# Optimization experiments

Hardware: AMD Instinct MI355X
Metric: run time of the kernel (lower is better)

## Reference

```python
import jax, jax.numpy as jnp
import numpy as np

D_MODEL, D_STATE, D_CONV, EXPAND, L = 512, 16, 4, 2, 2048
D_INNER = EXPAND * D_MODEL


def _dwconv_causal(x, w, b):
    # x: (L, D), w: (D, K), b: (D,). torch Conv1d(groups=D, padding=K-1)[..., :L]
    K = w.shape[1]
    xp = jnp.pad(x, ((K - 1, 0), (0, 0)))
    windows = jnp.stack([xp[k:k + x.shape[0]] for k in range(K)], axis=-1)  # (L, D, K)
    return jnp.einsum('ldk,dk->ld', windows, w) + b


def _ssm_dir(x, inW, inb, cw, cb, xpW, xpb, dtW, dtb, outW, outb, A_log, Dp):
    xz = x @ inW + inb                      # (L, 2*Di)
    x_ssm, z = xz[:, :D_INNER], xz[:, D_INNER:]
    x_ssm = _dwconv_causal(x_ssm, cw, cb)   # (L, Di)
    sp = jax.nn.silu(x_ssm) @ xpW + xpb     # (L, Di + 2*S)
    delta = sp[:, :D_INNER]
    B = sp[:, D_INNER:D_INNER + D_STATE]
    C = sp[:, D_INNER + D_STATE:]
    dt = jax.nn.softplus(delta @ dtW + dtb)  # (L, Di)
    A = -jnp.exp(A_log)                      # (Di, S)
    dA = jnp.exp(dt[:, :, None] * A[None])                      # (L, Di, S)
    dBu = dt[:, :, None] * B[:, None, :] * x_ssm[:, :, None]    # (L, Di, S)

    def step(h, inp):
        a, bu = inp
        h = a * h + bu
        return h, h

    h0 = jnp.zeros((D_INNER, D_STATE), x.dtype)
    _, hs = jax.lax.scan(step, h0, (dA, dBu))   # (L, Di, S)
    y = jnp.einsum('lds,ls->ld', hs, C) + Dp * x_ssm
    return (y * jax.nn.silu(z)) @ outW + outb


def _make_params(key):
    ks = jax.random.split(key, 32)
    i = iter(range(32))
    def w(shape, scale=0.02):
        return (jax.random.normal(ks[next(i)], shape, jnp.float32) * scale)
    p = {}
    for pre in ('fwd_', 'bwd_'):
        p[pre + 'in_W'] = w((D_MODEL, 2 * D_INNER))
        p[pre + 'in_b'] = w((2 * D_INNER,))
        p[pre + 'conv_w'] = w((D_INNER, D_CONV), 0.1)
        p[pre + 'conv_b'] = w((D_INNER,))
        p[pre + 'xp_W'] = w((D_INNER, D_INNER + 2 * D_STATE))
        p[pre + 'xp_b'] = w((D_INNER + 2 * D_STATE,))
        p[pre + 'dt_W'] = w((D_INNER, D_INNER))
        p[pre + 'dt_b'] = w((D_INNER,))
        p[pre + 'out_W'] = w((D_INNER, D_MODEL))
        p[pre + 'out_b'] = w((D_MODEL,))
    p['A_log'] = jax.random.normal(ks[next(i)], (D_INNER, D_STATE), jnp.float32) * 0.5
    p['D_param'] = jnp.ones((D_INNER,), jnp.float32)
    p['fusion_W'] = w((2 * D_MODEL, D_MODEL))
    p['fusion_b'] = w((D_MODEL,))
    return p


def setup_inputs() -> dict:
    key = jax.random.key(0)
    kx, kp = jax.random.split(key)
    inp = {'x': jax.random.normal(kx, (L, D_MODEL), jnp.float32)}
    inp.update(_make_params(kp))
    return inp


def reference(x,
              fwd_in_W, fwd_in_b, fwd_conv_w, fwd_conv_b, fwd_xp_W, fwd_xp_b,
              fwd_dt_W, fwd_dt_b, fwd_out_W, fwd_out_b,
              bwd_in_W, bwd_in_b, bwd_conv_w, bwd_conv_b, bwd_xp_W, bwd_xp_b,
              bwd_dt_W, bwd_dt_b, bwd_out_W, bwd_out_b,
              A_log, D_param, fusion_W, fusion_b):
    out_fwd = _ssm_dir(x, fwd_in_W, fwd_in_b, fwd_conv_w, fwd_conv_b,
                       fwd_xp_W, fwd_xp_b, fwd_dt_W, fwd_dt_b,
                       fwd_out_W, fwd_out_b, A_log, D_param)
    out_bwd = _ssm_dir(x[::-1], bwd_in_W, bwd_in_b, bwd_conv_w, bwd_conv_b,
                       bwd_xp_W, bwd_xp_b, bwd_dt_W, bwd_dt_b,
                       bwd_out_W, bwd_out_b, A_log, D_param)[::-1]
    return jnp.concatenate([out_fwd, out_bwd], axis=-1) @ fusion_W + fusion_b
```

## Files before the change

### kernel.cpp

```cpp
#include <hip/hip_runtime.h>
#include <cmath>

#define L_SEQ 2048
#define DM 512
#define DI 1024
#define DS 16
#define NSP 1056
#define NC 64
#define CL 32

typedef unsigned short ushortT;
typedef unsigned int u32;
typedef __attribute__((ext_vector_type(8))) short short8;
typedef __attribute__((ext_vector_type(4))) unsigned short ushort4_t;
typedef __attribute__((ext_vector_type(4))) float float4_t;
typedef __attribute__((address_space(1))) u32 gu32;
typedef __attribute__((address_space(3))) u32 lu32;

__device__ __forceinline__ float sigm(float x) { return 1.0f / (1.0f + __expf(-x)); }

__device__ __forceinline__ ushortT f2bf(float f) {
    unsigned u = __float_as_uint(f);
    unsigned r = u + 0x7FFFu + ((u >> 16) & 1u);
    return (ushortT)(r >> 16);
}
__device__ __forceinline__ float b2f(ushortT u) {
    return __uint_as_float(((u32)u) << 16);
}

__device__ __forceinline__ void gl2lds16(const ushortT* g, ushortT* l) {
    __builtin_amdgcn_global_load_lds((gu32*)g, (lu32*)l, 16, 0, 0);
}

struct WC {
    const float* src[11];
    ushortT* dst[11];
    int ss[11], soff[11], ds_[11], tN[11], mode[11];
    int off[12];
};

__global__ __launch_bounds__(256) void prep_all(
    WC wc, int nW,
    const float* __restrict__ x, ushortT* __restrict__ xb,
    const float* __restrict__ xpb0, const float* __restrict__ xpb1,
    const float* __restrict__ dtW0, const float* __restrict__ dtW1,
    const float* __restrict__ dtb0, const float* __restrict__ dtb1,
    const float* __restrict__ outb0, const float* __restrict__ outb1,
    const float* __restrict__ fuW, const float* __restrict__ fub,
    float* __restrict__ BFdt0, float* __restrict__ BFdt1, float* __restrict__ BFof)
{
    __shared__ ushortT t[32][33];
    __shared__ float red[256];
    int b = blockIdx.x;
    int tid = threadIdx.x;
    if (b < nW) {
        int m = 0;
        while (b >= wc.off[m + 1]) ++m;
        int tl = b - wc.off[m];
        int n0 = (tl % wc.tN[m]) * 32;
        int k0 = (tl / wc.tN[m]) * 32;
        const float* W = wc.src[m];
        ushortT* D = wc.dst[m];
        int ss = wc.ss[m], soff = wc.soff[m], ds = wc.ds_[m];
        int tx = tid & 31, ty = tid >> 5;
        if (wc.mode[m] == 1) {
            #pragma unroll
            for (int i = 0; i < 32; i += 8)
                D[(size_t)(k0 + ty + i) * ds + n0 + tx] =
                    f2bf(W[(size_t)(k0 + ty + i) * ss + soff + n0 + tx]);
        } else {
            #pragma unroll
            for (int i = 0; i < 32; i += 8)
                t[ty + i][tx] = f2bf(W[(size_t)(k0 + ty + i) * ss + soff + n0 + tx]);
            __syncthreads();
            #pragma unroll
            for (int i = 0; i < 32; i += 8)
                D[(size_t)(n0 + ty + i) * ds + k0 + tx] = t[tx][ty + i];
        }
        return;
    }
    b -= nW;
    if (b < 1024) {
        int i = (b * 256 + tid) * 4;
        float4_t v = *(const float4_t*)(x + i);
        xb[i + 0] = f2bf(v[0]); xb[i + 1] = f2bf(v[1]);
        xb[i + 2] = f2bf(v[2]); xb[i + 3] = f2bf(v[3]);
        return;
    }
    int o = b - 1024;
    float acc = 0.0f;
    if (o < 2112) {
        int dir = o >= 1056;
        int m = o - dir * 1056;
        const float* xpb = dir ? xpb1 : xpb0;
        float* BF = dir ? BFdt1 : BFdt0;
        if (m >= 1024) {
            if (tid == 0) BF[m] = xpb[m];
            return;
        }
        const float* dtW = dir ? dtW1 : dtW0;
        const float* dtb = dir ? dtb1 : dtb0;
        for (int n = tid; n < 1024; n += 256) acc += xpb[n] * dtW[n * 1024 + m];
        red[tid] = acc;
        __syncthreads();
        for (int s = 128; s > 0; s >>= 1) {
            if (tid < s) red[tid] += red[tid + s];
            __syncthreads();
        }
        if (tid == 0) BF[m] = red[0] + dtb[m];
    } else {
        int n = o - 2112;
        for (int j = tid; j < 1024; j += 256) {
            float ob = (j < 512) ? outb0[j] : outb1[j - 512];
            acc += ob * fuW[(size_t)j * 512 + n];
        }
        red[tid] = acc;
        __syncthreads();
        for (int s = 128; s > 0; s >>= 1) {
            if (tid < s) red[tid] += red[tid + s];
            __syncthreads();
        }
        if (tid == 0) BFof[n] = red[0] + fub[n];
    }
}

template<int BM, int BN>
__device__ __forceinline__ void gemm_core(
    ushortT* As, ushortT* Bs, int bm, int bn,
    const ushortT* __restrict__ A, int lda, int revA,
    const ushortT* __restrict__ A2, int dualK,
    const ushortT* __restrict__ W,
    const float* __restrict__ bias,
    float* __restrict__ Cf, int ldcf,
    float* __restrict__ Cf2, int ldcf2, int Nsplit,
    ushortT* __restrict__ Cb, int ldcb,
    ushortT* __restrict__ Cb2, int ldcb2,
    int M, int N, int K, int epi)
{
    constexpr int BK = 64;
    constexpr int MI = BM / 32;
    constexpr int NI = BN / 32;
    constexpr int CA = BM / 32;
    constexpr int CB = BN / 32;
    constexpr int ABUF = BM * BK;
    constexpr int BBUF = BN * BK;

    const int tid  = threadIdx.x;
    const int wave = tid >> 6;
    const int lane = tid & 63;
    const int quad = lane >> 4;
    const int r    = lane & 15;
    const int wm   = (wave >> 1) * (BM / 2);
    const int wn   = (wave & 1) * (BN / 2);

    const int lrow = lane >> 3;
    const int lk   = ((lane & 7) ^ lrow) * 8;

    const ushortT* gA[CA]; const ushortT* gA2[CA]; ushortT* lA[CA];
    #pragma unroll
    for (int c = 0; c < CA; ++c) {
        int row = bm + c * 32 + wave * 8 + lrow;
        int r0 = revA ? (M - 1 - row) : row;
        gA[c] = A + (size_t)r0 * lda + lk;
        gA2[c] = dualK ? (A2 + (size_t)(M - 1 - row) * lda + lk) : gA[c];
        lA[c] = &As[(c * 32 + wave * 8) * BK];
    }
    const ushortT* gB[CB]; ushortT* lB[CB];
    #pragma unroll
    for (int c = 0; c < CB; ++c) {
        int row = bn + c * 32 + wave * 8 + lrow;
        if (row > N - 1) row = N - 1;
        gB[c] = W + (size_t)row * K + lk;
        lB[c] = &Bs[(c * 32 + wave * 8) * BK];
    }

    float4_t acc[MI][NI];
    #pragma unroll
    for (int i = 0; i < MI; ++i)
        #pragma unroll
        for (int j = 0; j < NI; ++j)
            acc[i][j] = (float4_t){0.f, 0.f, 0.f, 0.f};

    const int nsteps = K >> 6;

    auto stage = [&](int step, int buf) {
        int kq = step << 6;
        #pragma unroll
        for (int c = 0; c < CA; ++c) {
            const ushortT* s = (!dualK || kq < 1024) ? gA[c] + kq : gA2[c] + (kq - 1024);
            gl2lds16(s, lA[c] + buf * ABUF);
        }
        #pragma unroll
        for (int c = 0; c < CB; ++c)
            gl2lds16(gB[c] + kq, lB[c] + buf * BBUF);
    };
    auto compute = [&](int buf) {
        #pragma unroll
        for (int kh = 0; kh < 2; ++kh) {
            const int slot = (((kh * 4 + quad) ^ (lane & 7)) * 8);
            short8 af[MI], bf[NI];
            #pragma unroll
            for (int mi = 0; mi < MI; ++mi)
                af[mi] = *(const short8*)&As[buf * ABUF + (wm + mi * 16 + r) * BK + slot];
            #pragma unroll
            for (int ni = 0; ni < NI; ++ni)
                bf[ni] = *(const short8*)&Bs[buf * BBUF + (wn + ni * 16 + r) * BK + slot];
            #pragma unroll
            for (int mi = 0; mi < MI; ++mi)
                #pragma unroll
                for (int ni = 0; ni < NI; ++ni)
                    acc[mi][ni] = __builtin_amdgcn_mfma_f32_16x16x32_bf16(
                        af[mi], bf[ni], acc[mi][ni], 0, 0, 0);
        }
    };

    stage(0, 0);
    for (int i = 0; i < nsteps; i += 2) {
        __syncthreads();
        if (i + 1 < nsteps) stage(i + 1, 1);
        compute(0);
        __syncthreads();
        if (i + 2 < nsteps) stage(i + 2, 0);
        compute(1);
    }

    #pragma unroll
    for (int mi = 0; mi < MI; ++mi) {
        int rowb = bm + wm + mi * 16 + quad * 4;
        #pragma unroll
        for (int ni = 0; ni < NI; ++ni) {
            int gn = bn + wn + ni * 16 + r;
            if (gn < N) {
                float bv = bias ? bias[gn] : 0.0f;
                #pragma unroll
                for (int j = 0; j < 4; ++j) {
                    int orow = rowb + j;
                    float v = acc[mi][ni][j] + bv;
                    if (gn < Nsplit) {
                        if (epi == 1) v = (v > 20.0f) ? v : log1pf(__expf(v));
                        if (Cf) Cf[(size_t)orow * ldcf + gn] = v;
                        if (Cb) Cb[(size_t)orow * ldcb + gn] = f2bf(v);
                    } else {
                        if (Cf2) Cf2[(size_t)orow * ldcf2 + gn - Nsplit] = v;
                        if (Cb2) Cb2[(size_t)orow * ldcb2 + gn - Nsplit] = f2bf(v);
                    }
                }
            }
        }
    }
}

__global__ __launch_bounds__(256) void mega_k(
    const ushortT* __restrict__ XB, const ushortT* __restrict__ WtIn,
    const float* __restrict__ inb0, const float* __restrict__ inb1,
    ushortT* __restrict__ XSb, ushortT* __restrict__ Zb,
    const ushortT* __restrict__ WtDt, const ushortT* __restrict__ XpD,
    ushortT* __restrict__ WtXpF,
    const ushortT* __restrict__ WtFu, const ushortT* __restrict__ OutC,
    ushortT* __restrict__ WtOF2)
{
    __shared__ ushortT As[2 * 128 * 64];
    __shared__ ushortT Bs[2 * 64 * 64];
    int z = blockIdx.z;
    if (z < 2) {
        long long b = ((long long)z * 16 + blockIdx.y) * 32 + blockIdx.x;
        int xc = (int)(b & 7);
        long long k = b >> 3;
        int dir = xc & 1;
        int q = xc >> 1;
        int bx = q * 8 + (int)(k % 8);
        int by = (int)(k / 8);
        gemm_core<128, 64>(As, Bs, by * 128, bx * 64,
            XB, DM, dir, nullptr, 0,
            WtIn + (size_t)dir * 2 * DI * DM,
            dir ? inb1 : inb0,
            nullptr, 0, nullptr, 0, DI,
            XSb + (size_t)dir * L_SEQ * DI, DI,
            Zb + (size_t)dir * L_SEQ * DI, DI,
            L_SEQ, 2 * DI, DM, 0);
    } else if (z < 4) {
        if (blockIdx.x >= 16) return;
        int d = z - 2;
        gemm_core<64, 64>(As, Bs, blockIdx.y * 64, blockIdx.x * 64,
            WtDt + (size_t)d * DI * DI, DI, 0, nullptr, 0,
            XpD + (size_t)d * DI * DI,
            nullptr, nullptr, 0, nullptr, 0, DI,
            WtXpF + (size_t)d * NSP * DI, DI, nullptr, 0,
            DI, DI, DI, 0);
    } else {
        if (blockIdx.x >= 16 || blockIdx.y >= 8) return;
        int d = z - 4;
        gemm_core<64, 64>(As, Bs, blockIdx.y * 64, blockIdx.x * 64,
            WtFu + (size_t)d * DM, DI, 0, nullptr, 0,
            OutC + (size_t)d * DI * DM,
            nullptr, nullptr, 0, nullptr, 0, DI,
            WtOF2 + (size_t)d * DI, 2 * DI, nullptr, 0,
            DM, DI, DM, 0);
    }
}

template<int BM, int BN>
__global__ __launch_bounds__(256) void gemm_bf16(
    const ushortT* __restrict__ A, int lda, long long Astr, int revAmode,
    const ushortT* __restrict__ W, long long Wstr,
    const float* __restrict__ bias0, const float* __restrict__ bias1,
    float* __restrict__ Cf, int ldcf, long long Cfstr,
    float* __restrict__ Cf2, int ldcf2, long long Cf2str, int Nsplit,
    ushortT* __restrict__ Cb, int ldcb, long long Cbstr,
    ushortT* __restrict__ Cb2, int ldcb2, long long Cb2str,
    int swz, int M, int N, int K, int epi)
{
    __shared__ ushortT As[2 * BM * 64];
    __shared__ ushortT Bs[2 * BN * 64];
    int bx = blockIdx.x, by = blockIdx.y, dir = blockIdx.z;
    if (swz) {
        int gx = gridDim.x, gy = gridDim.y, gz = gridDim.z;
        long long b = ((long long)dir * gy + by) * gx + bx;
        int xc = (int)(b & 7);
        long long k = b >> 3;
        if (gz == 2) {
            dir = xc & 1;
            int q = xc >> 1;
            if (swz == 1) { int qc = gx >> 2; bx = q * qc + (int)(k % qc); by = (int)(k / qc); }
            else          { int qc = gy >> 2; by = q * qc + (int)(k % qc); bx = (int)(k / qc); }
        } else {
            if (swz == 1) { int qc = gx >> 3; bx = xc * qc + (int)(k % qc); by = (int)(k / qc); }
            else          { int qc = gy >> 3; by = xc * qc + (int)(k % qc); bx = (int)(k / qc); }
        }
    }
    const ushortT* Ad = A;
    const ushortT* A2 = A;
    int revA = 0, dualK = 0;
    if (revAmode == 3) { dualK = 1; A2 = A + Astr; }
    else { Ad += (size_t)dir * Astr; revA = (revAmode == 2) ? dir : revAmode; }
    gemm_core<BM, BN>(As, Bs, by * BM, bx * BN,
        Ad, lda, revA, A2, dualK,
        W + (size_t)dir * Wstr,
        dir ? bias1 : bias0,
        Cf ? Cf + (size_t)dir * Cfstr : nullptr, ldcf,
        Cf2 ? Cf2 + (size_t)dir * Cf2str : nullptr, ldcf2, Nsplit,
        Cb ? Cb + (size_t)dir * Cbstr : nullptr, ldcb,
        Cb2 ? Cb2 + (size_t)dir * Cb2str : nullptr, ldcb2,
        M, N, K, epi);
}

__global__ __launch_bounds__(256) void conv_k(
    const ushortT* __restrict__ XSb,
    const float* __restrict__ cw0, const float* __restrict__ cw1,
    const float* __restrict__ cb0, const float* __restrict__ cb1,
    ushortT* __restrict__ SCb)
{
    int dir = blockIdx.z;
    XSb += (size_t)dir * L_SEQ * DI;
    SCb += (size_t)dir * L_SEQ * DI;
    const float* cw = dir ? cw1 : cw0;
    const float* cb = dir ? cb1 : cb0;
    int idx = (blockIdx.x * 256 + threadIdx.x) * 4;
    int d4 = idx & (DI - 1);
    int l = idx >> 10;
    ushort4_t r0 = *(const ushort4_t*)(XSb + (size_t)l * DI + d4);
    ushort4_t r1 = (l >= 1) ? *(const ushort4_t*)(XSb + (size_t)(l - 1) * DI + d4) : (ushort4_t){0,0,0,0};
    ushort4_t r2 = (l >= 2) ? *(const ushort4_t*)(XSb + (size_t)(l - 2) * DI + d4) : (ushort4_t){0,0,0,0};
    ushort4_t r3 = (l >= 3) ? *(const ushort4_t*)(XSb + (size_t)(l - 3) * DI + d4) : (ushort4_t){0,0,0,0};
    ushort4_t outv;
    #pragma unroll
    for (int j = 0; j < 4; ++j) {
        int d = d4 + j;
        float acc = cb[d] + cw[d * 4 + 0] * b2f(r3[j]) + cw[d * 4 + 1] * b2f(r2[j])
                  + cw[d * 4 + 2] * b2f(r1[j]) + cw[d * 4 + 3] * b2f(r0[j]);
        outv[j] = f2bf(acc * sigm(acc));
    }
    *(ushort4_t*)(SCb + idx) = outv;
}

__global__ __launch_bounds__(256) void scanA_k(
    const ushortT* __restrict__ DTb, const ushortT* __restrict__ XSb,
    const float* __restrict__ BC, const float* __restrict__ Alog,
    const float* __restrict__ cw0, const float* __restrict__ cw1,
    const float* __restrict__ cb0, const float* __restrict__ cb1,
    float* __restrict__ Pend, float* __restrict__ Hl)
{
    __shared__ float Bsh[CL][DS];
    int dir = blockIdx.z;
    int c = blockIdx.y;
    int d = blockIdx.x * 256 + threadIdx.x;
    DTb += (size_t)dir * L_SEQ * DI;
    XSb += (size_t)dir * L_SEQ * DI;
    BC  += (size_t)dir * L_SEQ * 32;
    const float* cw = dir ? cw1 : cw0;
    const float* cb = dir ? cb1 : cb0;
    int l0 = c * CL;
    for (int i = threadIdx.x; i < CL * DS; i += 256) {
        int ll = i >> 4, ss = i & 15;
        Bsh[ll][ss] = BC[(size_t)(l0 + ll) * 32 + ss];
    }
    __syncthreads();
    float w0 = cw[d * 4 + 0], w1 = cw[d * 4 + 1], w2 = cw[d * 4 + 2], w3 = cw[d * 4 + 3];
    float cbv = cb[d];
    float x3 = (l0 >= 3) ? b2f(XSb[(size_t)(l0 - 3) * DI + d]) : 0.f;
    float x2 = (l0 >= 2) ? b2f(XSb[(size_t)(l0 - 2) * DI + d]) : 0.f;
    float x1 = (l0 >= 1) ? b2f(XSb[(size_t)(l0 - 1) * DI + d]) : 0.f;
    float Ae[DS], h[DS], P[DS];
    #pragma unroll
    for (int s = 0; s < DS; ++s) { Ae[s] = -__expf(Alog[d * DS + s]); h[s] = 0.f; P[s] = 1.f; }
    for (int t = 0; t < CL; ++t) {
        int l = l0 + t;
        float x0 = b2f(XSb[(size_t)l * DI + d]);
        float xv = cbv + w0 * x3 + w1 * x2 + w2 * x1 + w3 * x0;
        x3 = x2; x2 = x1; x1 = x0;
        float dt = b2f(DTb[(size_t)l * DI + d]);
        float dtx = dt * xv;
        #pragma unroll
        for (int s = 0; s < DS; ++s) {
            float e = __expf(dt * Ae[s]);
            h[s] = e * h[s] + dtx * Bsh[t][s];
            P[s] *= e;
        }
    }
    size_t o = ((size_t)(dir * NC + c) * DI + d) * DS;
    #pragma unroll
    for (int s = 0; s < DS; ++s) { Pend[o + s] = P[s]; Hl[o + s] = h[s]; }
}

__global__ __launch_bounds__(256) void scanB_k(
    const float* __restrict__ Pend, const float* __restrict__ Hl, float* __restrict__ Hs)
{
    int idx = blockIdx.x * 256 + threadIdx.x;
    float h = 0.f;
    int ds = idx & 16383;
    int dir = idx >> 14;
    for (int c = 0; c < NC; ++c) {
        size_t o = ((size_t)(dir * NC + c)) * (DI * DS) + ds;
        Hs[o] = h;
        h = Pend[o] * h + Hl[o];
    }
}

__global__ __launch_bounds__(256) void scanC_k(
    const ushortT* __restrict__ DTb, const ushortT* __restrict__ XSb,
    const float* __restrict__ BC, const ushortT* __restrict__ Zb,
    const float* __restrict__ Alog, const float* __restrict__ Dp,
    const float* __restrict__ cw0, const float* __restrict__ cw1,
    const float* __restrict__ cb0, const float* __restrict__ cb1,
    const float* __restrict__ Hs, ushortT* __restrict__ Gb)
{
    __shared__ float Bsh[CL][DS];
    __shared__ float Csh[CL][DS];
    int dir = blockIdx.z;
    int c = blockIdx.y;
    int d = blockIdx.x * 256 + threadIdx.x;
    DTb += (size_t)dir * L_SEQ * DI;
    XSb += (size_t)dir * L_SEQ * DI;
    BC  += (size_t)dir * L_SEQ * 32;
    Zb  += (size_t)dir * L_SEQ * DI;
    Gb  += (size_t)dir * L_SEQ * DI;
    const float* cw = dir ? cw1 : cw0;
    const float* cb = dir ? cb1 : cb0;
    int l0 = c * CL;
    for (int i = threadIdx.x; i < CL * DS; i += 256) {
        int ll = i >> 4, ss = i & 15;
        size_t base = (size_t)(l0 + ll) * 32;
        Bsh[ll][ss] = BC[base + ss];
        Csh[ll][ss] = BC[base + DS + ss];
    }
    __syncthreads();
    float w0 = cw[d * 4 + 0], w1 = cw[d * 4 + 1], w2 = cw[d * 4 + 2], w3 = cw[d * 4 + 3];
    float cbv = cb[d];
    float x3 = (l0 >= 3) ? b2f(XSb[(size_t)(l0 - 3) * DI + d]) : 0.f;
    float x2 = (l0 >= 2) ? b2f(XSb[(size_t)(l0 - 2) * DI + d]) : 0.f;
    float x1 = (l0 >= 1) ? b2f(XSb[(size_t)(l0 - 1) * DI + d]) : 0.f;
    float Ae[DS], h[DS];
    size_t o = ((size_t)(dir * NC + c) * DI + d) * DS;
    #pragma unroll
    for (int s = 0; s < DS; ++s) { Ae[s] = -__expf(Alog[d * DS + s]); h[s] = Hs[o + s]; }
    float dpv = Dp[d];
    for (int t = 0; t < CL; ++t) {
        int l = l0 + t;
        float x0 = b2f(XSb[(size_t)l * DI + d]);
        float xv = cbv + w0 * x3 + w1 * x2 + w2 * x1 + w3 * x0;
        x3 = x2; x2 = x1; x1 = x0;
        float dt = b2f(DTb[(size_t)l * DI + d]);
        float dtx = dt * xv;
        float y = 0.f;
        #pragma unroll
        for (int s = 0; s < DS; ++s) {
            float e = __expf(dt * Ae[s]);
            h[s] = e * h[s] + dtx * Bsh[t][s];
            y += h[s] * Csh[t][s];
        }
        y += dpv * xv;
        float z = b2f(Zb[(size_t)l * DI + d]);
        Gb[(size_t)l * DI + d] = f2bf(y * (z * sigm(z)));
    }
}

extern "C" void kernel_launch(void* const* d_in, const int* in_sizes, int n_in,
                              void* d_out, int out_size, void* d_ws, size_t ws_size,
                              hipStream_t stream)
{
    (void)in_sizes; (void)n_in; (void)out_size; (void)ws_size;
    const float* x = (const float*)d_in[0];
    const float* inW[2]  = {(const float*)d_in[1],  (const float*)d_in[11]};
    const float* inb[2]  = {(const float*)d_in[2],  (const float*)d_in[12]};
    const float* cw[2]   = {(const float*)d_in[3],  (const float*)d_in[13]};
    const float* cb[2]   = {(const float*)d_in[4],  (const float*)d_in[14]};
    const float* xpW[2]  = {(const float*)d_in[5],  (const float*)d_in[15]};
    const float* xpb[2]  = {(const float*)d_in[6],  (const float*)d_in[16]};
    const float* dtW[2]  = {(const float*)d_in[7],  (const float*)d_in[17]};
// ... 22 lines not shown
    auto ualloc = [&](size_t n) { ushortT* p = wsu + uoff; uoff += n; return p; };
    ushortT* WtIn  = ualloc((size_t)2 * (2 * DI) * DM);
    ushortT* WtDt  = ualloc((size_t)2 * DI * DI);
    ushortT* WtFu  = ualloc((size_t)DM * DI);
    ushortT* WtXpF = ualloc((size_t)2 * NSP * DI);
    ushortT* XpD   = ualloc((size_t)2 * DI * DI);
    ushortT* OutC  = ualloc((size_t)2 * DI * DM);
    ushortT* WtOF2 = ualloc((size_t)DM * 2 * DI);
    ushortT* XB    = ualloc((size_t)L_SEQ * DM);
    ushortT* XSb   = ualloc((size_t)2 * L_SEQ * DI);
    ushortT* Zb    = ualloc((size_t)2 * L_SEQ * DI);
    ushortT* SCb   = ualloc((size_t)2 * L_SEQ * DI);
    ushortT* DTbB  = ualloc((size_t)2 * L_SEQ * DI);
    ushortT* Gb    = ualloc((size_t)2 * L_SEQ * DI);

    dim3 blk(256);

    WC wc;
    struct E { const float* s; ushortT* d; int ss, so, ds, N, K, mode; };
    E es[11] = {
        {inW[0],  WtIn,                          2 * DI, 0,    DM, 2 * DI, DM, 0},
        {inW[1],  WtIn + (size_t)2 * DI * DM,    2 * DI, 0,    DM, 2 * DI, DM, 0},
        {dtW[0],  WtDt,                          DI,     0,    DI, DI,     DI, 0},
        {dtW[1],  WtDt + (size_t)DI * DI,        DI,     0,    DI, DI,     DI, 0},
        {fuW,     WtFu,                          DM,     0,    DI, DM,     DI, 0},
        {xpW[0],  WtXpF + (size_t)DI * DI,       NSP,    DI,   DI, 32,     DI, 0},
        {xpW[1],  WtXpF + (size_t)NSP * DI + (size_t)DI * DI, NSP, DI, DI, 32, DI, 0},
        {xpW[0],  XpD,                           NSP,    0,    DI, DI,     DI, 1},
        {xpW[1],  XpD + (size_t)DI * DI,         NSP,    0,    DI, DI,     DI, 1},
        {outW[0], OutC,                          DM,     0,    DM, DM,     DI, 1},
        {outW[1], OutC + (size_t)DI * DM,        DM,     0,    DM, DM,     DI, 1},
    };
    wc.off[0] = 0;
    for (int m = 0; m < 11; ++m) {
        wc.src[m] = es[m].s; wc.dst[m] = es[m].d;
        wc.ss[m] = es[m].ss; wc.soff[m] = es[m].so; wc.ds_[m] = es[m].ds;
        wc.tN[m] = es[m].N / 32; wc.mode[m] = es[m].mode;
        wc.off[m + 1] = wc.off[m] + (es[m].N / 32) * (es[m].K / 32);
    }
    int nW = wc.off[11];
    prep_all<<<dim3(nW + 1024 + 2624), blk, 0, stream>>>(
        wc, nW, x, XB,
        xpb[0], xpb[1], dtW[0], dtW[1], dtb[0], dtb[1],
        outb[0], outb[1], fuW, fub, BFdt0, BFdt1, BFof);

    mega_k<<<dim3(32, 16, 6), blk, 0, stream>>>(
        XB, WtIn, inb[0], inb[1], XSb, Zb,
        WtDt, XpD, WtXpF, WtFu, OutC, WtOF2);

    conv_k<<<dim3(L_SEQ * DI / 1024, 1, 2), blk, 0, stream>>>(
        XSb, cw[0], cw[1], cb[0], cb[1], SCb);
    gemm_bf16<128, 64><<<dim3((NSP + 63) / 64, 16, 2), blk, 0, stream>>>(
        SCb, DI, (long long)L_SEQ * DI, 0, WtXpF, (long long)NSP * DI, BFdt0, BFdt1,
        nullptr, 0, 0, BCf, 32, (long long)L_SEQ * 32, DI,
        DTbB, DI, (long long)L_SEQ * DI, nullptr, 0, 0,
        2, L_SEQ, NSP, DI, 1);
    scanA_k<<<dim3(DI / 256, NC, 2), blk, 0, stream>>>(
        DTbB, XSb, BCf, Alog, cw[0], cw[1], cb[0], cb[1], Pend, Hl);
    scanB_k<<<dim3(2 * DI * DS / 256), blk, 0, stream>>>(Pend, Hl, Hs);
    scanC_k<<<dim3(DI / 256, NC, 2), blk, 0, stream>>>(
        DTbB, XSb, BCf, Zb, Alog, Dp, cw[0], cw[1], cb[0], cb[1], Hs, Gb);
    gemm_bf16<64, 32><<<dim3(DM / 32, 32, 1), blk, 0, stream>>>(
        Gb, DI, (long long)L_SEQ * DI, 3, WtOF2, 0, BFof, BFof,
        out, DM, 0, nullptr, 0, 0, DM,
        nullptr, 0, 0, nullptr, 0, 0,
        2, L_SEQ, DM, 2 * DI, 0);
}
```

Measured before the change: 318.2 us.

## Fuse all pipeline stages into one persistent cooperative kernel with grid syncs

Replaces the sequence of eight kernel launches (prep, input GEMMs, conv, x-proj GEMM, three scan phases, final GEMM) with a single persistent cooperative kernel. Blocks loop over job indices for each stage, separated by grid-wide barriers. The aim is to remove per-launch overhead and inter-kernel gaps. In exchange, the grid is capped by occupancy (2 blocks per CU via launch bounds), every stage shares one LDS allocation sized for the largest, and gemm_core is no longer force-inlined, all of which can reduce per-stage throughput. A fallback path launches separate kernels if the cooperative launch fails.

```diff
diff --git a/kernel.cpp b/kernel.cpp
--- a/kernel.cpp
+++ b/kernel.cpp
@@ -1,5 +1,8 @@
 #include <hip/hip_runtime.h>
+#include <hip/hip_cooperative_groups.h>
 #include <cmath>
+
+namespace cg = cooperative_groups;
 
 #define L_SEQ 2048
 #define DM 512
@@ -27,7 +30,6 @@
 __device__ __forceinline__ float b2f(ushortT u) {
     return __uint_as_float(((u32)u) << 16);
 }
-
 __device__ __forceinline__ void gl2lds16(const ushortT* g, ushortT* l) {
     __builtin_amdgcn_global_load_lds((gu32*)g, (lu32*)l, 16, 0, 0);
 }
@@ -39,21 +41,158 @@
     int off[12];
 };
 
-__global__ __launch_bounds__(256) void prep_all(
-    WC wc, int nW,
-    const float* __restrict__ x, ushortT* __restrict__ xb,
-    const float* __restrict__ xpb0, const float* __restrict__ xpb1,
-    const float* __restrict__ dtW0, const float* __restrict__ dtW1,
-    const float* __restrict__ dtb0, const float* __restrict__ dtb1,
-    const float* __restrict__ outb0, const float* __restrict__ outb1,
-    const float* __restrict__ fuW, const float* __restrict__ fub,
-    float* __restrict__ BFdt0, float* __restrict__ BFdt1, float* __restrict__ BFof)
-{
-    __shared__ ushortT t[32][33];
-    __shared__ float red[256];
-    int b = blockIdx.x;
+struct KP {
+    WC wc; int nW, nprep;
+    const float* x; ushortT* XB;
+    const float *xpb0, *xpb1, *dtW0, *dtW1, *dtb0, *dtb1;
+    const float *outb0, *outb1, *fuW, *fub;
+    float *BFdt0, *BFdt1, *BFof;
+    const float *inb0, *inb1;
+    ushortT *WtIn, *WtDt, *WtFu, *WtXpF, *XpD, *OutC, *WtOF2;
+    ushortT *XSb, *Zb, *SCb, *DTbB, *Gb;
+    float *BCf;
+    const float *cw0, *cw1, *cb0, *cb1;
+    const float *Alog, *Dp;
+    float *Pend, *Hl, *Hs;
+    float* out;
+};
+
+template<int BM, int BN>
+__device__ void gemm_core(
+    ushortT* As, ushortT* Bs, int bm, int bn,
+    const ushortT* __restrict__ A, int lda, int revA,
+    const ushortT* __restrict__ A2, int dualK,
+    const ushortT* __restrict__ W,
+    const float* __restrict__ bias,
+    float* __restrict__ Cf, int ldcf,
+    float* __restrict__ Cf2, int ldcf2, int Nsplit,
+    ushortT* __restrict__ Cb, int ldcb,
+    ushortT* __restrict__ Cb2, int ldcb2,
+    int M, int N, int K, int epi)
+{
+    constexpr int BK = 64;
+    constexpr int MI = BM / 32;
+    constexpr int NI = BN / 32;
+    constexpr int CA = BM / 32;
+    constexpr int CB = BN / 32;
+    constexpr int ABUF = BM * BK;
+    constexpr int BBUF = BN * BK;
+
+    __syncthreads();
+
+    const int tid  = threadIdx.x;
+    const int wave = tid >> 6;
+    const int lane = tid & 63;
+    const int quad = lane >> 4;
+    const int r    = lane & 15;
+    const int wm   = (wave >> 1) * (BM / 2);
+    const int wn   = (wave & 1) * (BN / 2);
+
+    const int lrow = lane >> 3;
+    const int lk   = ((lane & 7) ^ lrow) * 8;
+
+    const ushortT* gA[CA]; const ushortT* gA2[CA]; ushortT* lA[CA];
+    #pragma unroll
+    for (int c = 0; c < CA; ++c) {
+        int row = bm + c * 32 + wave * 8 + lrow;
+        int r0 = revA ? (M - 1 - row) : row;
+        gA[c] = A + (size_t)r0 * lda + lk;
+        gA2[c] = dualK ? (A2 + (size_t)(M - 1 - row) * lda + lk) : gA[c];
+        lA[c] = &As[(c * 32 + wave * 8) * BK];
+    }
+    const ushortT* gB[CB]; ushortT* lB[CB];
+    #pragma unroll
+    for (int c = 0; c < CB; ++c) {
+        int row = bn + c * 32 + wave * 8 + lrow;
+        if (row > N - 1) row = N - 1;
+        gB[c] = W + (size_t)row * K + lk;
+        lB[c] = &Bs[(c * 32 + wave * 8) * BK];
+    }
+
+    float4_t acc[MI][NI];
+    #pragma unroll
+    for (int i = 0; i < MI; ++i)
+        #pragma unroll
+        for (int j = 0; j < NI; ++j)
+            acc[i][j] = (float4_t){0.f, 0.f, 0.f, 0.f};
+
+    const int nsteps = K >> 6;
+
+    auto stage = [&](int step, int buf) {
+        int kq = step << 6;
+        #pragma unroll
+        for (int c = 0; c < CA; ++c) {
+            const ushortT* s = (!dualK || kq < 1024) ? gA[c] + kq : gA2[c] + (kq - 1024);
+            gl2lds16(s, lA[c] + buf * ABUF);
+        }
+        #pragma unroll
+        for (int c = 0; c < CB; ++c)
+            gl2lds16(gB[c] + kq, lB[c] + buf * BBUF);
+    };
+    auto compute = [&](int buf) {
+        #pragma unroll
+        for (int kh = 0; kh < 2; ++kh) {
+            const int slot = (((kh * 4 + quad) ^ (lane & 7)) * 8);
+            short8 af[MI], bf[NI];
+            #pragma unroll
+            for (int mi = 0; mi < MI; ++mi)
+                af[mi] = *(const short8*)&As[buf * ABUF + (wm + mi * 16 + r) * BK + slot];
+            #pragma unroll
+            for (int ni = 0; ni < NI; ++ni)
+                bf[ni] = *(const short8*)&Bs[buf * BBUF + (wn + ni * 16 + r) * BK + slot];
+            #pragma unroll
+            for (int mi = 0; mi < MI; ++mi)
+                #pragma unroll
+                for (int ni = 0; ni < NI; ++ni)
+                    acc[mi][ni] = __builtin_amdgcn_mfma_f32_16x16x32_bf16(
+                        af[mi], bf[ni], acc[mi][ni], 0, 0, 0);
+        }
+    };
+
+    stage(0, 0);
+    for (int i = 0; i < nsteps; i += 2) {
+        __syncthreads();
+        if (i + 1 < nsteps) stage(i + 1, 1);
+        compute(0);
+        __syncthreads();
+        if (i + 2 < nsteps) stage(i + 2, 0);
+        compute(1);
+    }
+
+    #pragma unroll
+    for (int mi = 0; mi < MI; ++mi) {
+        int rowb = bm + wm + mi * 16 + quad * 4;
+        #pragma unroll
+        for (int ni = 0; ni < NI; ++ni) {
+            int gn = bn + wn + ni * 16 + r;
+            if (gn < N) {
+                float bv = bias ? bias[gn] : 0.0f;
+                #pragma unroll
+                for (int j = 0; j < 4; ++j) {
+                    int orow = rowb + j;
+                    float v = acc[mi][ni][j] + bv;
+                    if (gn < Nsplit) {
+                        if (epi == 1) v = (v > 20.0f) ? v : log1pf(__expf(v));
+                        if (Cf) Cf[(size_t)orow * ldcf + gn] = v;
+                        if (Cb) Cb[(size_t)orow * ldcb + gn] = f2bf(v);
+                    } else {
+                        if (Cf2) Cf2[(size_t)orow * ldcf2 + gn - Nsplit] = v;
+                        if (Cb2) Cb2[(size_t)orow * ldcb2 + gn - Nsplit] = f2bf(v);
+                    }
+                }
+            }
+        }
+    }
+}
+
+__device__ void prep_job(const KP& p, int b, ushortT* smem)
+{
+    __syncthreads();
+    ushortT (*t)[33] = (ushortT(*)[33])smem;
+    float* red = (float*)(smem + 2112);
     int tid = threadIdx.x;
-    if (b < nW) {
+    if (b < p.nW) {
+        const WC& wc = p.wc;
         int m = 0;
         while (b >= wc.off[m + 1]) ++m;
         int tl = b - wc.off[m];
@@ -79,12 +218,12 @@
         }
         return;
     }
-    b -= nW;
+    b -= p.nW;
     if (b < 1024) {
         int i = (b * 256 + tid) * 4;
-        float4_t v = *(const float4_t*)(x + i);
-        xb[i + 0] = f2bf(v[0]); xb[i + 1] = f2bf(v[1]);
-        xb[i + 2] = f2bf(v[2]); xb[i + 3] = f2bf(v[3]);
+        float4_t v = *(const float4_t*)(p.x + i);
+        p.XB[i + 0] = f2bf(v[0]); p.XB[i + 1] = f2bf(v[1]);
+        p.XB[i + 2] = f2bf(v[2]); p.XB[i + 3] = f2bf(v[3]);
         return;
     }
     int o = b - 1024;
@@ -92,14 +231,14 @@
     if (o < 2112) {
         int dir = o >= 1056;
         int m = o - dir * 1056;
-        const float* xpb = dir ? xpb1 : xpb0;
-        float* BF = dir ? BFdt1 : BFdt0;
+        const float* xpb = dir ? p.xpb1 : p.xpb0;
+        float* BF = dir ? p.BFdt1 : p.BFdt0;
         if (m >= 1024) {
             if (tid == 0) BF[m] = xpb[m];
             return;
         }
-        const float* dtW = dir ? dtW1 : dtW0;
-        const float* dtb = dir ? dtb1 : dtb0;
+        const float* dtW = dir ? p.dtW1 : p.dtW0;
+        const float* dtb = dir ? p.dtb1 : p.dtb0;
         for (int n = tid; n < 1024; n += 256) acc += xpb[n] * dtW[n * 1024 + m];
         red[tid] = acc;
         __syncthreads();
@@ -111,8 +250,8 @@
     } else {
         int n = o - 2112;
         for (int j = tid; j < 1024; j += 256) {
-            float ob = (j < 512) ? outb0[j] : outb1[j - 512];
-            acc += ob * fuW[(size_t)j * 512 + n];
+            float ob = (j < 512) ? p.outb0[j] : p.outb1[j - 512];
+            acc += ob * p.fuW[(size_t)j * 512 + n];
         }
         red[tid] = acc;
         __syncthreads();
@@ -120,242 +259,59 @@
             if (tid < s) red[tid] += red[tid + s];
             __syncthreads();
         }
-        if (tid == 0) BFof[n] = red[0] + fub[n];
-    }
-}
-
-template<int BM, int BN>
-__device__ __forceinline__ void gemm_core(
-    ushortT* As, ushortT* Bs, int bm, int bn,
-    const ushortT* __restrict__ A, int lda, int revA,
-    const ushortT* __restrict__ A2, int dualK,
-    const ushortT* __restrict__ W,
-    const float* __restrict__ bias,
-    float* __restrict__ Cf, int ldcf,
-    float* __restrict__ Cf2, int ldcf2, int Nsplit,
-    ushortT* __restrict__ Cb, int ldcb,
-    ushortT* __restrict__ Cb2, int ldcb2,
-    int M, int N, int K, int epi)
-{
-    constexpr int BK = 64;
-    constexpr int MI = BM / 32;
-    constexpr int NI = BN / 32;
-    constexpr int CA = BM / 32;
-    constexpr int CB = BN / 32;
-    constexpr int ABUF = BM * BK;
-    constexpr int BBUF = BN * BK;
-
-    const int tid  = threadIdx.x;
-    const int wave = tid >> 6;
-    const int lane = tid & 63;
-    const int quad = lane >> 4;
-    const int r    = lane & 15;
-    const int wm   = (wave >> 1) * (BM / 2);
-    const int wn   = (wave & 1) * (BN / 2);
-
-    const int lrow = lane >> 3;
-    const int lk   = ((lane & 7) ^ lrow) * 8;
-
-    const ushortT* gA[CA]; const ushortT* gA2[CA]; ushortT* lA[CA];
-    #pragma unroll
-    for (int c = 0; c < CA; ++c) {
-        int row = bm + c * 32 + wave * 8 + lrow;
-        int r0 = revA ? (M - 1 - row) : row;
-        gA[c] = A + (size_t)r0 * lda + lk;
-        gA2[c] = dualK ? (A2 + (size_t)(M - 1 - row) * lda + lk) : gA[c];
-        lA[c] = &As[(c * 32 + wave * 8) * BK];
-    }
-    const ushortT* gB[CB]; ushortT* lB[CB];
-    #pragma unroll
-    for (int c = 0; c < CB; ++c) {
-        int row = bn + c * 32 + wave * 8 + lrow;
-        if (row > N - 1) row = N - 1;
-        gB[c] = W + (size_t)row * K + lk;
-        lB[c] = &Bs[(c * 32 + wave * 8) * BK];
-    }
-
-    float4_t acc[MI][NI];
-    #pragma unroll
-    for (int i = 0; i < MI; ++i)
-        #pragma unroll
-        for (int j = 0; j < NI; ++j)
-            acc[i][j] = (float4_t){0.f, 0.f, 0.f, 0.f};
-
-    const int nsteps = K >> 6;
-
-    auto stage = [&](int step, int buf) {
-        int kq = step << 6;
-        #pragma unroll
-        for (int c = 0; c < CA; ++c) {
-            const ushortT* s = (!dualK || kq < 1024) ? gA[c] + kq : gA2[c] + (kq - 1024);
-            gl2lds16(s, lA[c] + buf * ABUF);
-        }
-        #pragma unroll
-        for (int c = 0; c < CB; ++c)
-            gl2lds16(gB[c] + kq, lB[c] + buf * BBUF);
-    };
-    auto compute = [&](int buf) {
-        #pragma unroll
-        for (int kh = 0; kh < 2; ++kh) {
-            const int slot = (((kh * 4 + quad) ^ (lane & 7)) * 8);
-            short8 af[MI], bf[NI];
-            #pragma unroll
-            for (int mi = 0; mi < MI; ++mi)
-                af[mi] = *(const short8*)&As[buf * ABUF + (wm + mi * 16 + r) * BK + slot];
-            #pragma unroll
-            for (int ni = 0; ni < NI; ++ni)
-                bf[ni] = *(const short8*)&Bs[buf * BBUF + (wn + ni * 16 + r) * BK + slot];
-            #pragma unroll
-            for (int mi = 0; mi < MI; ++mi)
-                #pragma unroll
-                for (int ni = 0; ni < NI; ++ni)
-                    acc[mi][ni] = __builtin_amdgcn_mfma_f32_16x16x32_bf16(
-                        af[mi], bf[ni], acc[mi][ni], 0, 0, 0);
-        }
-    };
-
-    stage(0, 0);
-    for (int i = 0; i < nsteps; i += 2) {
-        __syncthreads();
-        if (i + 1 < nsteps) stage(i + 1, 1);
-        compute(0);
-        __syncthreads();
-        if (i + 2 < nsteps) stage(i + 2, 0);
-        compute(1);
-    }
-
-    #pragma unroll
-    for (int mi = 0; mi < MI; ++mi) {
-        int rowb = bm + wm + mi * 16 + quad * 4;
-        #pragma unroll
-        for (int ni = 0; ni < NI; ++ni) {
-            int gn = bn + wn + ni * 16 + r;
-            if (gn < N) {
-                float bv = bias ? bias[gn] : 0.0f;
-                #pragma unroll
-                for (int j = 0; j < 4; ++j) {
-                    int orow = rowb + j;
-                    float v = acc[mi][ni][j] + bv;
-                    if (gn < Nsplit) {
-                        if (epi == 1) v = (v > 20.0f) ? v : log1pf(__expf(v));
-                        if (Cf) Cf[(size_t)orow * ldcf + gn] = v;
-                        if (Cb) Cb[(size_t)orow * ldcb + gn] = f2bf(v);
-                    } else {
-                        if (Cf2) Cf2[(size_t)orow * ldcf2 + gn - Nsplit] = v;
-                        if (Cb2) Cb2[(size_t)orow * ldcb2 + gn - Nsplit] = f2bf(v);
-                    }
-                }
-            }
-        }
-    }
-}
-
-__global__ __launch_bounds__(256) void mega_k(
-    const ushortT* __restrict__ XB, const ushortT* __restrict__ WtIn,
-    const float* __restrict__ inb0, const float* __restrict__ inb1,
-    ushortT* __restrict__ XSb, ushortT* __restrict__ Zb,
-    const ushortT* __restrict__ WtDt, const ushortT* __restrict__ XpD,
-    ushortT* __restrict__ WtXpF,
-    const ushortT* __restrict__ WtFu, const ushortT* __restrict__ OutC,
-    ushortT* __restrict__ WtOF2)
-{
-    __shared__ ushortT As[2 * 128 * 64];
-    __shared__ ushortT Bs[2 * 64 * 64];
-    int z = blockIdx.z;
-    if (z < 2) {
-        long long b = ((long long)z * 16 + blockIdx.y) * 32 + blockIdx.x;
-        int xc = (int)(b & 7);
-        long long k = b >> 3;
+        if (tid == 0) p.BFof[n] = red[0] + p.fub[n];
+    }
+}
+
+__device__ void s1_job(const KP& p, int job, ushortT* As, ushortT* Bs)
+{
+    if (job < 1024) {
+        int xc = job & 7;
+        int k = job >> 3;
         int dir = xc & 1;
         int q = xc >> 1;
-        int bx = q * 8 + (int)(k % 8);
-        int by = (int)(k / 8);
+        int bx = q * 8 + (k & 7);
+        int by = k >> 3;
         gemm_core<128, 64>(As, Bs, by * 128, bx * 64,
-            XB, DM, dir, nullptr, 0,
-            WtIn + (size_t)dir * 2 * DI * DM,
-            dir ? inb1 : inb0,
+            p.XB, DM, dir, nullptr, 0,
+            p.WtIn + (size_t)dir * 2 * DI * DM,
+            dir ? p.inb1 : p.inb0,
             nullptr, 0, nullptr, 0, DI,
-            XSb + (size_t)dir * L_SEQ * DI, DI,
-            Zb + (size_t)dir * L_SEQ * DI, DI,
+            p.XSb + (size_t)dir * L_SEQ * DI, DI,
+            p.Zb + (size_t)dir * L_SEQ * DI, DI,
             L_SEQ, 2 * DI, DM, 0);
-    } else if (z < 4) {
-        if (blockIdx.x >= 16) return;
-        int d = z - 2;
-        gemm_core<64, 64>(As, Bs, blockIdx.y * 64, blockIdx.x * 64,
-            WtDt + (size_t)d * DI * DI, DI, 0, nullptr, 0,
-            XpD + (size_t)d * DI * DI,
+    } else if (job < 1536) {
+        int j = job - 1024;
+        int d = j >> 8;
+        int t = j & 255;
+        gemm_core<64, 64>(As, Bs, (t >> 4) * 64, (t & 15) * 64,
+            p.WtDt + (size_t)d * DI * DI, DI, 0, nullptr, 0,
+            p.XpD + (size_t)d * DI * DI,
             nullptr, nullptr, 0, nullptr, 0, DI,
-            WtXpF + (size_t)d * NSP * DI, DI, nullptr, 0,
+            p.WtXpF + (size_t)d * NSP * DI, DI, nullptr, 0,
             DI, DI, DI, 0);
     } else {
-        if (blockIdx.x >= 16 || blockIdx.y >= 8) return;
-        int d = z - 4;
-        gemm_core<64, 64>(As, Bs, blockIdx.y * 64, blockIdx.x * 64,
-            WtFu + (size_t)d * DM, DI, 0, nullptr, 0,
-            OutC + (size_t)d * DI * DM,
+        int j = job - 1536;
+        int d = j >> 7;
+        int t = j & 127;
+        gemm_core<64, 64>(As, Bs, (t >> 4) * 64, (t & 15) * 64,
+            p.WtFu + (size_t)d * DM, DI, 0, nullptr, 0,
+            p.OutC + (size_t)d * DI * DM,
             nullptr, nullptr, 0, nullptr, 0, DI,
-            WtOF2 + (size_t)d * DI, 2 * DI, nullptr, 0,
+            p.WtOF2 + (size_t)d * DI, 2 * DI, nullptr, 0,
             DM, DI, DM, 0);
     }
 }
 
-template<int BM, int BN>
-__global__ __launch_bounds__(256) void gemm_bf16(
-    const ushortT* __restrict__ A, int lda, long long Astr, int revAmode,
-    const ushortT* __restrict__ W, long long Wstr,
-    const float* __restrict__ bias0, const float* __restrict__ bias1,
-    float* __restrict__ Cf, int ldcf, long long Cfstr,
-    float* __restrict__ Cf2, int ldcf2, long long Cf2str, int Nsplit,
-    ushortT* __restrict__ Cb, int ldcb, long long Cbstr,
-    ushortT* __restrict__ Cb2, int ldcb2, long long Cb2str,
-    int swz, int M, int N, int K, int epi)
-{
-    __shared__ ushortT As[2 * BM * 64];
-    __shared__ ushortT Bs[2 * BN * 64];
-    int bx = blockIdx.x, by = blockIdx.y, dir = blockIdx.z;
-    if (swz) {
-        int gx = gridDim.x, gy = gridDim.y, gz = gridDim.z;
-        long long b = ((long long)dir * gy + by) * gx + bx;
-        int xc = (int)(b & 7);
-        long long k = b >> 3;
-        if (gz == 2) {
-            dir = xc & 1;
-            int q = xc >> 1;
-            if (swz == 1) { int qc = gx >> 2; bx = q * qc + (int)(k % qc); by = (int)(k / qc); }
-            else          { int qc = gy >> 2; by = q * qc + (int)(k % qc); bx = (int)(k / qc); }
-        } else {
-            if (swz == 1) { int qc = gx >> 3; bx = xc * qc + (int)(k % qc); by = (int)(k / qc); }
-            else          { int qc = gy >> 3; by = xc * qc + (int)(k % qc); bx = (int)(k / qc); }
-        }
-    }
-    const ushortT* Ad = A;
-    const ushortT* A2 = A;
-    int revA = 0, dualK = 0;
-    if (revAmode == 3) { dualK = 1; A2 = A + Astr; }
-    else { Ad += (size_t)dir * Astr; revA = (revAmode == 2) ? dir : revAmode; }
-    gemm_core<BM, BN>(As, Bs, by * BM, bx * BN,
-        Ad, lda, revA, A2, dualK,
-        W + (size_t)dir * Wstr,
-        dir ? bias1 : bias0,
-        Cf ? Cf + (size_t)dir * Cfstr : nullptr, ldcf,
-        Cf2 ? Cf2 + (size_t)dir * Cf2str : nullptr, ldcf2, Nsplit,
-        Cb ? Cb + (size_t)dir * Cbstr : nullptr, ldcb,
-        Cb2 ? Cb2 + (size_t)dir * Cb2str : nullptr, ldcb2,
-        M, N, K, epi);
-}
-
-__global__ __launch_bounds__(256) void conv_k(
-    const ushortT* __restrict__ XSb,
-    const float* __restrict__ cw0, const float* __restrict__ cw1,
-    const float* __restrict__ cb0, const float* __restrict__ cb1,
-    ushortT* __restrict__ SCb)
-{
-    int dir = blockIdx.z;
-    XSb += (size_t)dir * L_SEQ * DI;
-    SCb += (size_t)dir * L_SEQ * DI;
-    const float* cw = dir ? cw1 : cw0;
-    const float* cb = dir ? cb1 : cb0;
-    int idx = (blockIdx.x * 256 + threadIdx.x) * 4;
+__device__ void conv_job(const KP& p, int job)
+{
+    int dir = job >> 11;
+    int bx = job & 2047;
+    const ushortT* XSb = p.XSb + (size_t)dir * L_SEQ * DI;
+    ushortT* SCb = p.SCb + (size_t)dir * L_SEQ * DI;
+    const float* cw = dir ? p.cw1 : p.cw0;
+    const float* cb = dir ? p.cb1 : p.cb0;
+    int idx = (bx * 256 + threadIdx.x) * 4;
     int d4 = idx & (DI - 1);
     int l = idx >> 10;
     ushort4_t r0 = *(const ushort4_t*)(XSb + (size_t)l * DI + d4);
@@ -373,22 +329,36 @@
     *(ushort4_t*)(SCb + idx) = outv;
 }
 
-__global__ __launch_bounds__(256) void scanA_k(
-    const ushortT* __restrict__ DTb, const ushortT* __restrict__ XSb,
-    const float* __restrict__ BC, const float* __restrict__ Alog,
-    const float* __restrict__ cw0, const float* __restrict__ cw1,
-    const float* __restrict__ cb0, const float* __restrict__ cb1,
-    float* __restrict__ Pend, float* __restrict__ Hl)
-{
-    __shared__ float Bsh[CL][DS];
-    int dir = blockIdx.z;
-    int c = blockIdx.y;
-    int d = blockIdx.x * 256 + threadIdx.x;
-    DTb += (size_t)dir * L_SEQ * DI;
-    XSb += (size_t)dir * L_SEQ * DI;
-    BC  += (size_t)dir * L_SEQ * 32;
-    const float* cw = dir ? cw1 : cw0;
-    const float* cb = dir ? cb1 : cb0;
+__device__ void xp_job(const KP& p, int job, ushortT* As, ushortT* Bs)
+{
+    int xc = job & 7;
+    int k = job >> 3;
+    int dir = xc & 1;
+    int mq = xc >> 1;
+    int bx = k >> 2;
+    int by = mq * 4 + (k & 3);
+    gemm_core<128, 64>(As, Bs, by * 128, bx * 64,
+        p.SCb + (size_t)dir * L_SEQ * DI, DI, 0, nullptr, 0,
+        p.WtXpF + (size_t)dir * NSP * DI,
+        dir ? p.BFdt1 : p.BFdt0,
+        nullptr, 0,
+        p.BCf + (size_t)dir * L_SEQ * 32, 32, DI,
+        p.DTbB + (size_t)dir * L_SEQ * DI, DI, nullptr, 0,
+        L_SEQ, NSP, DI, 1);
+}
+
+__device__ void scanA_job(const KP& p, int job, float* fsh)
+{
+    __syncthreads();
+    float (*Bsh)[DS] = (float(*)[DS])fsh;
+    int dir = job >> 8;
+    int c = (job & 255) >> 2;
+    int d = (job & 3) * 256 + threadIdx.x;
+    const ushortT* DTb = p.DTbB + (size_t)dir * L_SEQ * DI;
+    const ushortT* XSb = p.XSb + (size_t)dir * L_SEQ * DI;
+    const float* BC = p.BCf + (size_t)dir * L_SEQ * 32;
+    const float* cw = dir ? p.cw1 : p.cw0;
+    const float* cb = dir ? p.cb1 : p.cb0;
     int l0 = c * CL;
     for (int i = threadIdx.x; i < CL * DS; i += 256) {
         int ll = i >> 4, ss = i & 15;
@@ -402,7 +372,7 @@
     float x1 = (l0 >= 1) ? b2f(XSb[(size_t)(l0 - 1) * DI + d]) : 0.f;
     float Ae[DS], h[DS], P[DS];
     #pragma unroll
-    for (int s = 0; s < DS; ++s) { Ae[s] = -__expf(Alog[d * DS + s]); h[s] = 0.f; P[s] = 1.f; }
+    for (int s = 0; s < DS; ++s) { Ae[s] = -__expf(p.Alog[d * DS + s]); h[s] = 0.f; P[s] = 1.f; }
     for (int t = 0; t < CL; ++t) {
         int l = l0 + t;
         float x0 = b2f(XSb[(size_t)l * DI + d]);
@@ -419,43 +389,37 @@
     }
     size_t o = ((size_t)(dir * NC + c) * DI + d) * DS;
     #pragma unroll
-    for (int s = 0; s < DS; ++s) { Pend[o + s] = P[s]; Hl[o + s] = h[s]; }
-}
-
-__global__ __launch_bounds__(256) void scanB_k(
-    const float* __restrict__ Pend, const float* __restrict__ Hl, float* __restrict__ Hs)
-{
-    int idx = blockIdx.x * 256 + threadIdx.x;
+    for (int s = 0; s < DS; ++s) { p.Pend[o + s] = P[s]; p.Hl[o + s] = h[s]; }
+}
+
+__device__ void scanB_job(const KP& p, int job)
+{
+    int idx = job * 256 + threadIdx.x;
     float h = 0.f;
     int ds = idx & 16383;
     int dir = idx >> 14;
     for (int c = 0; c < NC; ++c) {
         size_t o = ((size_t)(dir * NC + c)) * (DI * DS) + ds;
-        Hs[o] = h;
-        h = Pend[o] * h + Hl[o];
-    }
-}
-
-__global__ __launch_bounds__(256) void scanC_k(
-    const ushortT* __restrict__ DTb, const ushortT* __restrict__ XSb,
-    const float* __restrict__ BC, const ushortT* __restrict__ Zb,
-    const float* __restrict__ Alog, const float* __restrict__ Dp,
-    const float* __restrict__ cw0, const float* __restrict__ cw1,
-    const float* __restrict__ cb0, const float* __restrict__ cb1,
-    const float* __restrict__ Hs, ushortT* __restrict__ Gb)
-{
-    __shared__ float Bsh[CL][DS];
-    __shared__ float Csh[CL][DS];
-    int dir = blockIdx.z;
-    int c = blockIdx.y;
-    int d = blockIdx.x * 256 + threadIdx.x;
-    DTb += (size_t)dir * L_SEQ * DI;
-    XSb += (size_t)dir * L_SEQ * DI;
-    BC  += (size_t)dir * L_SEQ * 32;
-    Zb  += (size_t)dir * L_SEQ * DI;
-    Gb  += (size_t)dir * L_SEQ * DI;
-    const float* cw = dir ? cw1 : cw0;
-    const float* cb = dir ? cb1 : cb0;
+        p.Hs[o] = h;
+        h = p.Pend[o] * h + p.Hl[o];
+    }
+}
+
+__device__ void scanC_job(const KP& p, int job, float* fsh)
+{
+    __syncthreads();
+    float (*Bsh)[DS] = (float(*)[DS])fsh;
+    float (*Csh)[DS] = (float(*)[DS])(fsh + CL * DS);
+    int dir = job >> 8;
+    int c = (job & 255) >> 2;
+    int d = (job & 3) * 256 + threadIdx.x;
+    const ushortT* DTb = p.DTbB + (size_t)dir * L_SEQ * DI;
+    const ushortT* XSb = p.XSb + (size_t)dir * L_SEQ * DI;
+    const float* BC = p.BCf + (size_t)dir * L_SEQ * 32;
+    const ushortT* Zb = p.Zb + (size_t)dir * L_SEQ * DI;
+    ushortT* Gb = p.Gb + (size_t)dir * L_SEQ * DI;
+    const float* cw = dir ? p.cw1 : p.cw0;
+    const float* cb = dir ? p.cb1 : p.cb0;
     int l0 = c * CL;
     for (int i = threadIdx.x; i < CL * DS; i += 256) {
         int ll = i >> 4, ss = i & 15;
@@ -472,8 +436,8 @@
     float Ae[DS], h[DS];
     size_t o = ((size_t)(dir * NC + c) * DI + d) * DS;
     #pragma unroll
-    for (int s = 0; s < DS; ++s) { Ae[s] = -__expf(Alog[d * DS + s]); h[s] = Hs[o + s]; }
-    float dpv = Dp[d];
+    for (int s = 0; s < DS; ++s) { Ae[s] = -__expf(p.Alog[d * DS + s]); h[s] = p.Hs[o + s]; }
+    float dpv = p.Dp[d];
     for (int t = 0; t < CL; ++t) {
         int l = l0 + t;
         float x0 = b2f(XSb[(size_t)l * DI + d]);
@@ -492,6 +456,79 @@
         float z = b2f(Zb[(size_t)l * DI + d]);
         Gb[(size_t)l * DI + d] = f2bf(y * (z * sigm(z)));
     }
+}
+
+__device__ void final_job(const KP& p, int job, ushortT* As, ushortT* Bs)
+{
+    int xc = job & 7;
+    int k = job >> 3;
+    int by = xc * 4 + (k & 3);
+    int bx = k >> 2;
+    gemm_core<64, 32>(As, Bs, by * 64, bx * 32,
+        p.Gb, DI, 0, p.Gb + (size_t)L_SEQ * DI, 1,
+        p.WtOF2, p.BFof,
+        p.out, DM, nullptr, 0, DM,
+        nullptr, 0, nullptr, 0,
+        L_SEQ, DM, 2 * DI, 0);
+}
+
+__global__ __launch_bounds__(256, 2) void fused_k(KP p)
+{
+    __shared__ ushortT smem[24576];
+    ushortT* As = smem;
+    ushortT* Bs = smem + 16384;
+    cg::grid_group grid = cg::this_grid();
+    const int nb = gridDim.x;
+    const int b0 = blockIdx.x;
+
+    for (int job = b0; job < p.nprep; job += nb) prep_job(p, job, smem);
+    grid.sync();
+    for (int job = b0; job < 1792; job += nb) s1_job(p, job, As, Bs);
+    grid.sync();
+    for (int job = b0; job < 4096; job += nb) conv_job(p, job);
+    grid.sync();
+    for (int job = b0; job < 544; job += nb) xp_job(p, job, As, Bs);
+    grid.sync();
+    for (int job = b0; job < 512; job += nb) scanA_job(p, job, (float*)smem);
+    grid.sync();
+    for (int job = b0; job < 128; job += nb) scanB_job(p, job);
+    grid.sync();
+    for (int job = b0; job < 512; job += nb) scanC_job(p, job, (float*)smem);
+    grid.sync();
+    for (int job = b0; job < 512; job += nb) final_job(p, job, As, Bs);
+}
+
+__global__ __launch_bounds__(256) void prep_k(KP p)
+{
+    __shared__ ushortT smem[2624];
+    prep_job(p, blockIdx.x, smem);
+}
+__global__ __launch_bounds__(256) void s1_k(KP p)
+{
+    __shared__ ushortT smem[24576];
+    s1_job(p, blockIdx.x, smem, smem + 16384);
+}
+__global__ __launch_bounds__(256) void conv_sk(KP p) { conv_job(p, blockIdx.x); }
+__global__ __launch_bounds__(256) void xp_sk(KP p)
+{
+    __shared__ ushortT smem[24576];
+    xp_job(p, blockIdx.x, smem, smem + 16384);
+}
+__global__ __launch_bounds__(256) void scanA_sk(KP p)
+{
+    __shared__ float fsh[CL * DS];
+    scanA_job(p, blockIdx.x, fsh);
+}
+__global__ __launch_bounds__(256) void scanB_sk(KP p) { scanB_job(p, blockIdx.x); }
+__global__ __launch_bounds__(256) void scanC_sk(KP p)
+{
+    __shared__ float fsh[2 * CL * DS];
+    scanC_job(p, blockIdx.x, fsh);
+}
+__global__ __launch_bounds__(256) void final_sk(KP p)
+{
+    __shared__ ushortT smem[24576];
+    final_job(p, blockIdx.x, smem, smem + 16384);
 }
 
 extern "C" void kernel_launch(void* const* d_in, const int* in_sizes, int n_in,
@@ -544,9 +581,7 @@
     ushortT* DTbB  = ualloc((size_t)2 * L_SEQ * DI);
     ushortT* Gb    = ualloc((size_t)2 * L_SEQ * DI);
 
-    dim3 blk(256);
-
-    WC wc;
+    KP p;
     struct E { const float* s; ushortT* d; int ss, so, ds, N, K, mode; };
     E es[11] = {
         {inW[0],  WtIn,                          2 * DI, 0,    DM, 2 * DI, DM, 0},
@@ -561,38 +596,52 @@
         {outW[0], OutC,                          DM,     0,    DM, DM,     DI, 1},
         {outW[1], OutC + (size_t)DI * DM,        DM,     0,    DM, DM,     DI, 1},
     };
-    wc.off[0] = 0;
+    p.wc.off[0] = 0;
     for (int m = 0; m < 11; ++m) {
-        wc.src[m] = es[m].s; wc.dst[m] = es[m].d;
-        wc.ss[m] = es[m].ss; wc.soff[m] = es[m].so; wc.ds_[m] = es[m].ds;
-        wc.tN[m] = es[m].N / 32; wc.mode[m] = es[m].mode;
-        wc.off[m + 1] = wc.off[m] + (es[m].N / 32) * (es[m].K / 32);
-    }
-    int nW = wc.off[11];
-    prep_all<<<dim3(nW + 1024 + 2624), blk, 0, stream>>>(
-        wc, nW, x, XB,
-        xpb[0], xpb[1], dtW[0], dtW[1], dtb[0], dtb[1],
-        outb[0], outb[1], fuW, fub, BFdt0, BFdt1, BFof);
-
-    mega_k<<<dim3(32, 16, 6), blk, 0, stream>>>(
-        XB, WtIn, inb[0], inb[1], XSb, Zb,
-        WtDt, XpD, WtXpF, WtFu, OutC, WtOF2);
-
-    conv_k<<<dim3(L_SEQ * DI / 1024, 1, 2), blk, 0, stream>>>(
-        XSb, cw[0], cw[1], cb[0], cb[1], SCb);
-    gemm_bf16<128, 64><<<dim3((NSP + 63) / 64, 16, 2), blk, 0, stream>>>(
-        SCb, DI, (long long)L_SEQ * DI, 0, WtXpF, (long long)NSP * DI, BFdt0, BFdt1,
-        nullptr, 0, 0, BCf, 32, (long long)L_SEQ * 32, DI,
-        DTbB, DI, (long long)L_SEQ * DI, nullptr, 0, 0,
-        2, L_SEQ, NSP, DI, 1);
-    scanA_k<<<dim3(DI / 256, NC, 2), blk, 0, stream>>>(
-        DTbB, XSb, BCf, Alog, cw[0], cw[1], cb[0], cb[1], Pend, Hl);
-    scanB_k<<<dim3(2 * DI * DS / 256), blk, 0, stream>>>(Pend, Hl, Hs);
-    scanC_k<<<dim3(DI / 256, NC, 2), blk, 0, stream>>>(
-        DTbB, XSb, BCf, Zb, Alog, Dp, cw[0], cw[1], cb[0], cb[1], Hs, Gb);
-    gemm_bf16<64, 32><<<dim3(DM / 32, 32, 1), blk, 0, stream>>>(
-        Gb, DI, (long long)L_SEQ * DI, 3, WtOF2, 0, BFof, BFof,
-        out, DM, 0, nullptr, 0, 0, DM,
-        nullptr, 0, 0, nullptr, 0, 0,
-        2, L_SEQ, DM, 2 * DI, 0);
-}
+        p.wc.src[m] = es[m].s; p.wc.dst[m] = es[m].d;
+        p.wc.ss[m] = es[m].ss; p.wc.soff[m] = es[m].so; p.wc.ds_[m] = es[m].ds;
+        p.wc.tN[m] = es[m].N / 32; p.wc.mode[m] = es[m].mode;
+        p.wc.off[m + 1] = p.wc.off[m] + (es[m].N / 32) * (es[m].K / 32);
+    }
+    p.nW = p.wc.off[11];
+    p.nprep = p.nW + 1024 + 2624;
+    p.x = x; p.XB = XB;
+    p.xpb0 = xpb[0]; p.xpb1 = xpb[1];
+    p.dtW0 = dtW[0]; p.dtW1 = dtW[1];
+    p.dtb0 = dtb[0]; p.dtb1 = dtb[1];
+    p.outb0 = outb[0]; p.outb1 = outb[1];
+    p.fuW = fuW; p.fub = fub;
+    p.BFdt0 = BFdt0; p.BFdt1 = BFdt1; p.BFof = BFof;
+    p.inb0 = inb[0]; p.inb1 = inb[1];
+    p.WtIn = WtIn; p.WtDt = WtDt; p.WtFu = WtFu; p.WtXpF = WtXpF;
+    p.XpD = XpD; p.OutC = OutC; p.WtOF2 = WtOF2;
+    p.XSb = XSb; p.Zb = Zb; p.SCb = SCb; p.DTbB = DTbB; p.Gb = Gb;
+    p.BCf = BCf;
+    p.cw0 = cw[0]; p.cw1 = cw[1]; p.cb0 = cb[0]; p.cb1 = cb[1];
+    p.Alog = Alog; p.Dp = Dp;
+    p.Pend = Pend; p.Hl = Hl; p.Hs = Hs;
+    p.out = out;
+
+    hipError_t le = hipErrorUnknown;
+    int occ = 0;
+    if (hipOccupancyMaxActiveBlocksPerMultiprocessor(&occ, fused_k, 256, 0) == hipSuccess
+        && occ > 0) {
+        int nb = occ * 256;
+        if (nb > 1792) nb = 1792;
+        void* args[] = { &p };
+        le = hipLaunchCooperativeKernel(reinterpret_cast<void*>(fused_k),
+                                        dim3(nb), dim3(256), args, 0, stream);
+    }
+    if (le != hipSuccess) {
+        (void)hipGetLastError();
+        dim3 blk(256);
+        prep_k  <<<dim3(p.nprep), blk, 0, stream>>>(p);
+        s1_k    <<<dim3(1792),    blk, 0, stream>>>(p);
+        conv_sk <<<dim3(4096),    blk, 0, stream>>>(p);
+        xp_sk   <<<dim3(544),     blk, 0, stream>>>(p);
+        scanA_sk<<<dim3(512),     blk, 0, stream>>>(p);
+        scanB_sk<<<dim3(128),     blk, 0, stream>>>(p);
+        scanC_sk<<<dim3(512),     blk, 0, stream>>>(p);
+        final_sk<<<dim3(512),     blk, 0, stream>>>(p);
+    }
+}
```

Measured after the change: 671.4 us. +111.0%, slower.
